# Kernel tuning notes

Hardware: AMD Instinct MI355X
Metric: run time of the kernel (lower is better)

The kernel has to match this reference:

```python
import jax, jax.numpy as jnp
import numpy as np

D = 256  # feature_dim
B, N = 16, 1024
NEG_SLOPE = 0.2
SCALE = float(np.sqrt(D))


def setup_inputs() -> dict:
    key = jax.random.key(0)
    ks = jax.random.split(key, 8)
    s = 1.0 / np.sqrt(D)  # torch Linear default init scale
    return {
        "feature": jax.random.normal(ks[0], (B, N, D), dtype=jnp.float32),
        "graph": jax.random.randint(ks[1], (B, N, N), 0, 2, dtype=jnp.int32),
        "W_w": jax.random.uniform(ks[2], (D, D), jnp.float32, -s, s),
        "W_b": jax.random.uniform(ks[3], (D,), jnp.float32, -s, s),
        "Q_w": jax.random.uniform(ks[4], (D, D), jnp.float32, -s, s),
        "Q_b": jax.random.uniform(ks[5], (D,), jnp.float32, -s, s),
        "K_w": jax.random.uniform(ks[6], (D, D), jnp.float32, -s, s),
        "K_b": jax.random.uniform(ks[7], (D,), jnp.float32, -s, s),
    }


def reference(feature, graph, W_w, W_b, Q_w, Q_b, K_w, K_b):
    # h = W(feature); torch Linear: x @ W.T + b
    h = jnp.einsum('bnd,ed->bne', feature, W_w) + W_b        # [B,N,D]
    q = jnp.einsum('bnd,ed->bne', h, Q_w) + Q_b              # [B,N,D]
    k = jnp.einsum('bnd,ed->bne', h, K_w) + K_b              # [B,N,D]
    e = jnp.einsum('bnd,bmd->bnm', q, k) / SCALE             # [B,N,N]
    e = jnp.where(e >= 0, e, NEG_SLOPE * e)                  # LeakyReLU(0.2)
    e = jnp.where(graph == 0, jnp.float32(-1e9), e)          # mask
    a = jax.nn.softmax(e, axis=2)                            # dropout = identity (eval)
    out = jax.nn.relu(jnp.einsum('bnm,bmd->bnd', a, h))      # [B,N,D]
    return out
```

## Files before the change

kernel.cpp:

```cpp
#include <hip/hip_runtime.h>
#include <hip/hip_bf16.h>
#include <stdint.h>

#define DD 256
#define NB 16
#define NN 1024
#define MTOT (NB * NN)

typedef __attribute__((ext_vector_type(8))) short short8;
typedef __attribute__((ext_vector_type(4))) float f32x4;

__device__ __forceinline__ ushort f2b(float f) {
  uint32_t u = __float_as_uint(f);
  return (ushort)((u + 0x7fffu + ((u >> 16) & 1u)) >> 16);
}

__device__ __forceinline__ void stage_weights(const float* __restrict__ W,
                                              ushort* Wl, int tid) {
  for (int i = 0; i < 64; ++i) {
    int idx4 = i * 256 + tid;
    int row = idx4 >> 6;
    int col0 = (idx4 & 63) << 2;
    float4 v = ((const float4*)W)[idx4];
    ushort4 b4;
    b4.x = f2b(v.x); b4.y = f2b(v.y); b4.z = f2b(v.z); b4.w = f2b(v.w);
    int byte = (row * 512 + col0 * 2) ^ ((row & 7) << 4);
    *(ushort4*)((char*)Wl + byte) = b4;
  }
}

__global__ __launch_bounds__(256, 1) void gemm_fused(
    const float* __restrict__ feature, const float* __restrict__ W_w,
    const float* __restrict__ W_b, const float* __restrict__ Q_w,
    const float* __restrict__ Q_b, const float* __restrict__ K_w,
    const float* __restrict__ K_b, ushort* __restrict__ hT,
    ushort* __restrict__ q, ushort* __restrict__ k) {
  __shared__ ushort Wl[256 * 256];
  const int tid = threadIdx.x;
  const int w = tid >> 6, lane = tid & 63, l15 = lane & 15, hi = lane >> 4;
  const int m0 = blockIdx.x * 64 + w * 16;
  const int arow = m0 + l15;

  stage_weights(W_w, Wl, tid);
  __syncthreads();

  f32x4 acc[16] = {};
#pragma unroll
  for (int kk = 0; kk < 8; ++kk) {
    const int k0 = kk * 32 + hi * 8;
    const float4* ap = (const float4*)(feature + arow * 256 + k0);
    float4 x = ap[0], y = ap[1];
    short8 a;
    a[0] = (short)f2b(x.x); a[1] = (short)f2b(x.y);
    a[2] = (short)f2b(x.z); a[3] = (short)f2b(x.w);
    a[4] = (short)f2b(y.x); a[5] = (short)f2b(y.y);
    a[6] = (short)f2b(y.z); a[7] = (short)f2b(y.w);
#pragma unroll
    for (int et = 0; et < 16; ++et) {
      int er = et * 16 + l15;
      short8 bf = *(const short8*)((const char*)Wl +
                                   ((er * 512 + k0 * 2) ^ ((er & 7) << 4)));
      acc[et] = __builtin_amdgcn_mfma_f32_16x16x32_bf16(a, bf, acc[et], 0, 0, 0);
    }
  }

  ushort hvals[16][4];
#pragma unroll
  for (int et = 0; et < 16; ++et) {
    float bv = W_b[et * 16 + l15];
#pragma unroll
    for (int r = 0; r < 4; ++r) hvals[et][r] = f2b(acc[et][r] + bv);
  }

  __syncthreads();
  ushort* Tl = Wl;
  {
    const int mloc = w * 16 + hi * 4;
#pragma unroll
    for (int et = 0; et < 16; ++et)
#pragma unroll
      for (int r = 0; r < 4; ++r)
        Tl[(et * 16 + l15) * 64 + mloc + r] = hvals[et][r];
  }
  __syncthreads();

  short8 qa[8];
#pragma unroll
  for (int kk = 0; kk < 8; ++kk) {
    const int k0 = kk * 32 + hi * 8;
#pragma unroll
    for (int j = 0; j < 8; ++j)
      qa[kk][j] = (short)Tl[(k0 + j) * 64 + w * 16 + l15];
  }
  {
    const int bidx = blockIdx.x >> 4;
    const int n0 = (blockIdx.x & 15) * 64;
    ushort* dst = hT + bidx * (256 * 1024) + tid * 1024 + n0;
    const uint4* src = (const uint4*)(Tl + tid * 64);
#pragma unroll
    for (int j = 0; j < 8; ++j) ((uint4*)dst)[j] = src[j];
  }
  __syncthreads();

  stage_weights(Q_w, Wl, tid);
  __syncthreads();
#pragma unroll
  for (int et = 0; et < 16; ++et) acc[et] = (f32x4){0.f, 0.f, 0.f, 0.f};
#pragma unroll
  for (int kk = 0; kk < 8; ++kk) {
    const int k0 = kk * 32 + hi * 8;
#pragma unroll
    for (int et = 0; et < 16; ++et) {
      int er = et * 16 + l15;
      short8 bf = *(const short8*)((const char*)Wl +
                                   ((er * 512 + k0 * 2) ^ ((er & 7) << 4)));
      acc[et] = __builtin_amdgcn_mfma_f32_16x16x32_bf16(qa[kk], bf, acc[et], 0, 0, 0);
    }
  }
#pragma unroll
  for (int et = 0; et < 16; ++et) {
    int e = et * 16 + l15;
    float bv = Q_b[e];
#pragma unroll
    for (int r = 0; r < 4; ++r)
      q[(m0 + hi * 4 + r) * 256 + e] = f2b(acc[et][r] + bv);
  }
  __syncthreads();

  stage_weights(K_w, Wl, tid);
  __syncthreads();
#pragma unroll
  for (int et = 0; et < 16; ++et) acc[et] = (f32x4){0.f, 0.f, 0.f, 0.f};
#pragma unroll
  for (int kk = 0; kk < 8; ++kk) {
    const int k0 = kk * 32 + hi * 8;
#pragma unroll
    for (int et = 0; et < 16; ++et) {
      int er = et * 16 + l15;
      short8 bf = *(const short8*)((const char*)Wl +
                                   ((er * 512 + k0 * 2) ^ ((er & 7) << 4)));
      acc[et] = __builtin_amdgcn_mfma_f32_16x16x32_bf16(qa[kk], bf, acc[et], 0, 0, 0);
    }
  }
#pragma unroll
  for (int et = 0; et < 16; ++et) {
    int e = et * 16 + l15;
    float bv = K_b[e];
#pragma unroll
    for (int r = 0; r < 4; ++r)
      k[(m0 + hi * 4 + r) * 256 + e] = f2b(acc[et][r] + bv);
  }
}

#define SM_KT 0
#define SM_HT 32768
#define SM_PL 65536
#define SM_M2 73728
#define SM_CM 74752
#define SM_SZ 75008

__device__ __forceinline__ int pswz(int row, int bytecol) {
  return (row * 64 + bytecol) ^ ((row & 7) << 4) ^ ((row >> 3) << 5);
}

__global__ __launch_bounds__(512, 2) void attn8(
    const ushort* __restrict__ Q, const ushort* __restrict__ Kb,
    const ushort* __restrict__ HT, const int* __restrict__ graph,
    float* __restrict__ out) {
  __shared__ __align__(16) char smem[SM_SZ];
  ushort* Kt = (ushort*)(smem + SM_KT);
  ushort* Ht = (ushort*)(smem + SM_HT);
  ushort* Pl = (ushort*)(smem + SM_PL);
  uint* M2 = (uint*)(smem + SM_M2);
  float* Cm = (float*)(smem + SM_CM);

  const int tid = threadIdx.x;
  const int w = tid >> 6, lane = tid & 63, l15 = lane & 15, hi = lane >> 4;
  const int wg = w >> 1, half = w & 1;
  const int hw = blockIdx.x;
  const int slot = hw >> 3;
  const int b = (hw & 7) * 2 + (slot >> 4);
  const int q0 = (slot & 15) * 64;
  const int qrow_a = q0 + wg * 16 + l15;
  const int qrow_cl = wg * 16 + hi * 4;
  const int* grow_base = graph + (b * 1024 + q0 + w * 8) * 1024 + lane;

  int greg[8];

#pragma unroll
  for (int j = 0; j < 8; ++j) greg[j] = grow_base[j * 1024];

  short8 qf[8];
#pragma unroll
  for (int kk = 0; kk < 8; ++kk)
    qf[kk] = *(const short8*)(Q + (b * 1024 + qrow_a) * 256 + kk * 32 + hi * 8);

#pragma unroll
  for (int j = 0; j < 8; ++j) {
    unsigned long long mm = __ballot(greg[j] != 0);
    if (lane == 0) {
      M2[(w * 8 + j) * 2] = (uint)mm;
      M2[(w * 8 + j) * 2 + 1] = (uint)(mm >> 32);
    }
  }

  float lR[4] = {0.f, 0.f, 0.f, 0.f};
  f32x4 o[16] = {};

  for (int t = 0; t < 16; ++t) {
    const uint* M2c = M2 + (t & 1) * 128;
    uint* M2n = M2 + ((t & 1) ^ 1) * 128;

    __syncthreads();
#pragma unroll
    for (int i = 0; i < 4; ++i) {
      int c = i * 512 + tid;
      int krow = c >> 5, col0 = (c & 31) << 3;
      uint4 v = *(const uint4*)(Kb + (b * 1024 + t * 64 + krow) * 256 + col0);
      *(uint4*)((char*)Kt + ((krow * 512 + col0 * 2) ^ ((krow & 7) << 4))) = v;
    }
#pragma unroll
    for (int i = 0; i < 4; ++i) {
      int c = i * 512 + tid;
      int drow = c >> 3, col0 = (c & 7) << 3;
      uint4 v = *(const uint4*)(HT + b * (256 * 1024) + drow * 1024 + t * 64 + col0);
      *(uint4*)((char*)Ht + ((drow * 128 + col0 * 2) ^ ((drow & 7) << 4))) = v;
    }
    __syncthreads();

    if (t < 15) {
#pragma unroll
      for (int j = 0; j < 8; ++j) greg[j] = grow_base[j * 1024 + (t + 1) * 64];
    }

    f32x4 s[2] = {};
    __builtin_amdgcn_s_setprio(1);
#pragma unroll
    for (int kk = 0; kk < 8; ++kk) {
#pragma unroll
      for (int nt = 0; nt < 2; ++nt) {
        int krow = half * 32 + nt * 16 + l15;
        short8 kf = *(const short8*)((const char*)Kt +
            ((krow * 512 + (kk * 32 + hi * 8) * 2) ^ ((krow & 7) << 4)));
        s[nt] = __builtin_amdgcn_mfma_f32_16x16x32_bf16(qf[kk], kf, s[nt], 0, 0, 0);
      }
    }
    __builtin_amdgcn_s_setprio(0);

    float p[2][4];
#pragma unroll
    for (int r = 0; r < 4; ++r) {
      uint mw = M2c[(qrow_cl + r) * 2 + half];
      float v0 = s[0][r] * 0.0625f; v0 = (v0 >= 0.f) ? v0 : 0.2f * v0;
      float v1 = s[1][r] * 0.0625f; v1 = (v1 >= 0.f) ? v1 : 0.2f * v1;
      float p0 = ((mw >> l15) & 1u) ? __expf(v0) : 0.f;
      float p1 = ((mw >> (16 + l15)) & 1u) ? __expf(v1) : 0.f;
      p[0][r] = p0; p[1][r] = p1;
      lR[r] += p0 + p1;
    }

    ushort* Pw = Pl + w * 512;
#pragma unroll
    for (int nt = 0; nt < 2; ++nt)
#pragma unroll
      for (int r = 0; r < 4; ++r) {
        int row = hi * 4 + r, col = nt * 16 + l15;
        *(ushort*)((char*)Pw + pswz(row, col * 2)) = f2b(p[nt][r]);
      }
    __asm__ volatile("s_waitcnt lgkmcnt(0)" ::: "memory");
    short8 pa = *(const short8*)((const char*)Pw + pswz(l15, hi * 16));

    __builtin_amdgcn_s_setprio(1);
#pragma unroll
    for (int dt = 0; dt < 16; ++dt) {
      int dcol = dt * 16 + l15;
      short8 hf = *(const short8*)((const char*)Ht +
          ((dcol * 128 + (half * 32 + hi * 8) * 2) ^ ((dcol & 7) << 4)));
      o[dt] = __builtin_amdgcn_mfma_f32_16x16x32_bf16(pa, hf, o[dt], 0, 0, 0);
    }
    __builtin_amdgcn_s_setprio(0);

    if (t < 15) {
#pragma unroll
      for (int j = 0; j < 8; ++j) {
        unsigned long long mm = __ballot(greg[j] != 0);
        if (lane == 0) {
          M2n[(w * 8 + j) * 2] = (uint)mm;
          M2n[(w * 8 + j) * 2 + 1] = (uint)(mm >> 32);
        }
      }
    }
  }

#pragma unroll
  for (int r = 0; r < 4; ++r) {
    lR[r] += __shfl_xor(lR[r], 1);
    lR[r] += __shfl_xor(lR[r], 2);
    lR[r] += __shfl_xor(lR[r], 4);
    lR[r] += __shfl_xor(lR[r], 8);
  }

  __syncthreads();
  float* Ob = (float*)smem;
  if (half == 1) {
#pragma unroll
    for (int dt = 0; dt < 16; ++dt)
#pragma unroll
      for (int r = 0; r < 4; ++r) {
        int row = hi * 4 + r;
        int byte = (row * 1024 + (dt * 16 + l15) * 4) ^ ((row & 15) << 6);
        *(float*)((char*)Ob + wg * 16384 + byte) = o[dt][r];
      }
    if (l15 == 0) {
#pragma unroll
      for (int r = 0; r < 4; ++r)
        Cm[wg * 16 + hi * 4 + r] = lR[r];
    }
  }
  __syncthreads();
  if (half == 0) {
#pragma unroll
    for (int r = 0; r < 4; ++r) {
      int rowl = hi * 4 + r;
      float inv = 1.f / (lR[r] + Cm[wg * 16 + rowl]);
      int orow = b * 1024 + q0 + wg * 16 + rowl;
#pragma unroll
      for (int dt = 0; dt < 16; ++dt) {
        int byte = (rowl * 1024 + (dt * 16 + l15) * 4) ^ ((rowl & 15) << 6);
        float ob = *(const float*)((const char*)Ob + wg * 16384 + byte);
        float v = (o[dt][r] + ob) * inv;
        out[orow * 256 + dt * 16 + l15] = fmaxf(v, 0.f);
      }
    }
  }
}

extern "C" void kernel_launch(void* const* d_in, const int* in_sizes, int n_in,
                              void* d_out, int out_size, void* d_ws,
                              size_t ws_size, hipStream_t stream) {
  const float* feature = (const float*)d_in[0];
  const int* graph = (const int*)d_in[1];
  const float* W_w = (const float*)d_in[2];
  const float* W_b = (const float*)d_in[3];
  const float* Q_w = (const float*)d_in[4];
  const float* Q_b = (const float*)d_in[5];
  const float* K_w = (const float*)d_in[6];
  const float* K_b = (const float*)d_in[7];
  float* out = (float*)d_out;

  ushort* hT = (ushort*)d_ws;
  ushort* q = hT + MTOT * DD;
  ushort* k = q + MTOT * DD;

  gemm_fused<<<256, 256, 0, stream>>>(feature, W_w, W_b, Q_w, Q_b, K_w, K_b,
                                      hT, q, k);
  attn8<<<256, 512, 0, stream>>>(q, k, hT, graph, out);
}
```

Before: 93.69 us.

## Load K, H and graph mask directly from global memory, dropping LDS staging

The attention kernel no longer stages K and H^T tiles through shared memory with block-wide barriers. Each wave now reads its MFMA operand fragments straight from global memory (relying on L1/L2), and reads the graph mask per element instead of ballot-packing it into LDS bitmasks. This removes two __syncthreads per tile and the LDS copy traffic, at the cost of redundant global loads across waves, less coalesced 16-byte accesses, and no prefetch overlap for the next tile.

After: 166.2 us. +77.4%, slower.

```diff
diff --git a/kernel.cpp b/kernel.cpp
--- a/kernel.cpp
+++ b/kernel.cpp
@@ -152,12 +152,10 @@
   }
 }
 
-#define SM_KT 0
-#define SM_HT 32768
+#define SM_OB 0
 #define SM_PL 65536
-#define SM_M2 73728
-#define SM_CM 74752
-#define SM_SZ 75008
+#define SM_CM 73728
+#define SM_SZ 73984
 
 __device__ __forceinline__ int pswz(int row, int bytecol) {
   return (row * 64 + bytecol) ^ ((row & 7) << 4) ^ ((row >> 3) << 5);
@@ -168,10 +166,7 @@
     const ushort* __restrict__ HT, const int* __restrict__ graph,
     float* __restrict__ out) {
   __shared__ __align__(16) char smem[SM_SZ];
-  ushort* Kt = (ushort*)(smem + SM_KT);
-  ushort* Ht = (ushort*)(smem + SM_HT);
   ushort* Pl = (ushort*)(smem + SM_PL);
-  uint* M2 = (uint*)(smem + SM_M2);
   float* Cm = (float*)(smem + SM_CM);
 
   const int tid = threadIdx.x;
@@ -183,55 +178,26 @@
   const int q0 = (slot & 15) * 64;
   const int qrow_a = q0 + wg * 16 + l15;
   const int qrow_cl = wg * 16 + hi * 4;
-  const int* grow_base = graph + (b * 1024 + q0 + w * 8) * 1024 + lane;
-
-  int greg[8];
-
-#pragma unroll
-  for (int j = 0; j < 8; ++j) greg[j] = grow_base[j * 1024];
 
   short8 qf[8];
 #pragma unroll
   for (int kk = 0; kk < 8; ++kk)
     qf[kk] = *(const short8*)(Q + (b * 1024 + qrow_a) * 256 + kk * 32 + hi * 8);
 
-#pragma unroll
-  for (int j = 0; j < 8; ++j) {
-    unsigned long long mm = __ballot(greg[j] != 0);
-    if (lane == 0) {
-      M2[(w * 8 + j) * 2] = (uint)mm;
-      M2[(w * 8 + j) * 2 + 1] = (uint)(mm >> 32);
-    }
-  }
+  const ushort* Kbase = Kb + (b * 1024 + half * 32 + l15) * 256 + hi * 8;
+  const ushort* Hbase = HT + b * 262144 + half * 32 + hi * 8;
+  const int* Gbase = graph + (b * 1024 + q0 + qrow_cl) * 1024 + half * 32 + l15;
 
   float lR[4] = {0.f, 0.f, 0.f, 0.f};
   f32x4 o[16] = {};
 
   for (int t = 0; t < 16; ++t) {
-    const uint* M2c = M2 + (t & 1) * 128;
-    uint* M2n = M2 + ((t & 1) ^ 1) * 128;
-
-    __syncthreads();
-#pragma unroll
-    for (int i = 0; i < 4; ++i) {
-      int c = i * 512 + tid;
-      int krow = c >> 5, col0 = (c & 31) << 3;
-      uint4 v = *(const uint4*)(Kb + (b * 1024 + t * 64 + krow) * 256 + col0);
-      *(uint4*)((char*)Kt + ((krow * 512 + col0 * 2) ^ ((krow & 7) << 4))) = v;
-    }
-#pragma unroll
-    for (int i = 0; i < 4; ++i) {
-      int c = i * 512 + tid;
-      int drow = c >> 3, col0 = (c & 7) << 3;
-      uint4 v = *(const uint4*)(HT + b * (256 * 1024) + drow * 1024 + t * 64 + col0);
-      *(uint4*)((char*)Ht + ((drow * 128 + col0 * 2) ^ ((drow & 7) << 4))) = v;
-    }
-    __syncthreads();
-
-    if (t < 15) {
-#pragma unroll
-      for (int j = 0; j < 8; ++j) greg[j] = grow_base[j * 1024 + (t + 1) * 64];
-    }
+    int g[2][4];
+#pragma unroll
+    for (int nt = 0; nt < 2; ++nt)
+#pragma unroll
+      for (int r = 0; r < 4; ++r)
+        g[nt][r] = Gbase[r * 1024 + t * 64 + nt * 16];
 
     f32x4 s[2] = {};
     __builtin_amdgcn_s_setprio(1);
@@ -239,9 +205,7 @@
     for (int kk = 0; kk < 8; ++kk) {
 #pragma unroll
       for (int nt = 0; nt < 2; ++nt) {
-        int krow = half * 32 + nt * 16 + l15;
-        short8 kf = *(const short8*)((const char*)Kt +
-            ((krow * 512 + (kk * 32 + hi * 8) * 2) ^ ((krow & 7) << 4)));
+        short8 kf = *(const short8*)(Kbase + (t * 64 + nt * 16) * 256 + kk * 32);
         s[nt] = __builtin_amdgcn_mfma_f32_16x16x32_bf16(qf[kk], kf, s[nt], 0, 0, 0);
       }
     }
@@ -250,11 +214,10 @@
     float p[2][4];
 #pragma unroll
     for (int r = 0; r < 4; ++r) {
-      uint mw = M2c[(qrow_cl + r) * 2 + half];
       float v0 = s[0][r] * 0.0625f; v0 = (v0 >= 0.f) ? v0 : 0.2f * v0;
       float v1 = s[1][r] * 0.0625f; v1 = (v1 >= 0.f) ? v1 : 0.2f * v1;
-      float p0 = ((mw >> l15) & 1u) ? __expf(v0) : 0.f;
-      float p1 = ((mw >> (16 + l15)) & 1u) ? __expf(v1) : 0.f;
+      float p0 = g[0][r] ? __expf(v0) : 0.f;
+      float p1 = g[1][r] ? __expf(v1) : 0.f;
       p[0][r] = p0; p[1][r] = p1;
       lR[r] += p0 + p1;
     }
@@ -274,22 +237,10 @@
 #pragma unroll
     for (int dt = 0; dt < 16; ++dt) {
       int dcol = dt * 16 + l15;
-      short8 hf = *(const short8*)((const char*)Ht +
-          ((dcol * 128 + (half * 32 + hi * 8) * 2) ^ ((dcol & 7) << 4)));
+      short8 hf = *(const short8*)(Hbase + dcol * 1024 + t * 64);
       o[dt] = __builtin_amdgcn_mfma_f32_16x16x32_bf16(pa, hf, o[dt], 0, 0, 0);
     }
     __builtin_amdgcn_s_setprio(0);
-
-    if (t < 15) {
-#pragma unroll
-      for (int j = 0; j < 8; ++j) {
-        unsigned long long mm = __ballot(greg[j] != 0);
-        if (lane == 0) {
-          M2n[(w * 8 + j) * 2] = (uint)mm;
-          M2n[(w * 8 + j) * 2 + 1] = (uint)(mm >> 32);
-        }
-      }
-    }
   }
 
 #pragma unroll
@@ -300,8 +251,7 @@
     lR[r] += __shfl_xor(lR[r], 8);
   }
 
-  __syncthreads();
-  float* Ob = (float*)smem;
+  float* Ob = (float*)(smem + SM_OB);
   if (half == 1) {
 #pragma unroll
     for (int dt = 0; dt < 16; ++dt)
```

## Process 128 keys per outer iteration with doubled K/H LDS tiles

Applied to the files above, without the earlier changes.

Each outer iteration of the attention kernel now loads two 64-key chunks of K and H^T into separate LDS buffers. It then computes both sub-tiles before the next barrier, which halves the number of __syncthreads and loop iterations. LDS use roughly doubles to about 141KB, so launch bounds drop to one 512-thread block per CU. That reduces occupancy and latency hiding. Graph mask prefetch is widened to match.

After: 110.3 us. 1.18x slower.

```diff
diff --git a/kernel.cpp b/kernel.cpp
--- a/kernel.cpp
+++ b/kernel.cpp
@@ -152,24 +152,24 @@
   }
 }
 
-#define SM_KT 0
-#define SM_HT 32768
-#define SM_PL 65536
-#define SM_M2 73728
-#define SM_CM 74752
-#define SM_SZ 75008
+#define SM_KT0 0
+#define SM_KT1 32768
+#define SM_HT0 65536
+#define SM_HT1 98304
+#define SM_PL 131072
+#define SM_M2 139264
+#define SM_CM 141312
+#define SM_SZ 141568
 
 __device__ __forceinline__ int pswz(int row, int bytecol) {
   return (row * 64 + bytecol) ^ ((row & 7) << 4) ^ ((row >> 3) << 5);
 }
 
-__global__ __launch_bounds__(512, 2) void attn8(
+__global__ __launch_bounds__(512, 1) void attn8(
     const ushort* __restrict__ Q, const ushort* __restrict__ Kb,
     const ushort* __restrict__ HT, const int* __restrict__ graph,
     float* __restrict__ out) {
   __shared__ __align__(16) char smem[SM_SZ];
-  ushort* Kt = (ushort*)(smem + SM_KT);
-  ushort* Ht = (ushort*)(smem + SM_HT);
   ushort* Pl = (ushort*)(smem + SM_PL);
   uint* M2 = (uint*)(smem + SM_M2);
   float* Cm = (float*)(smem + SM_CM);
@@ -185,10 +185,13 @@
   const int qrow_cl = wg * 16 + hi * 4;
   const int* grow_base = graph + (b * 1024 + q0 + w * 8) * 1024 + lane;
 
-  int greg[8];
-
-#pragma unroll
-  for (int j = 0; j < 8; ++j) greg[j] = grow_base[j * 1024];
+  int greg[16];
+
+#pragma unroll
+  for (int j = 0; j < 8; ++j) {
+    greg[j] = grow_base[j * 1024];
+    greg[8 + j] = grow_base[j * 1024 + 64];
+  }
 
   short8 qf[8];
 #pragma unroll
@@ -197,96 +200,119 @@
 
 #pragma unroll
   for (int j = 0; j < 8; ++j) {
-    unsigned long long mm = __ballot(greg[j] != 0);
+    unsigned long long m0 = __ballot(greg[j] != 0);
+    unsigned long long m1 = __ballot(greg[8 + j] != 0);
     if (lane == 0) {
-      M2[(w * 8 + j) * 2] = (uint)mm;
-      M2[(w * 8 + j) * 2 + 1] = (uint)(mm >> 32);
+      M2[(w * 8 + j) * 2] = (uint)m0;
+      M2[(w * 8 + j) * 2 + 1] = (uint)(m0 >> 32);
+      M2[128 + (w * 8 + j) * 2] = (uint)m1;
+      M2[128 + (w * 8 + j) * 2 + 1] = (uint)(m1 >> 32);
     }
   }
 
   float lR[4] = {0.f, 0.f, 0.f, 0.f};
   f32x4 o[16] = {};
 
-  for (int t = 0; t < 16; ++t) {
-    const uint* M2c = M2 + (t & 1) * 128;
-    uint* M2n = M2 + ((t & 1) ^ 1) * 128;
+  for (int t = 0; t < 8; ++t) {
+    const int par = t & 1;
+    const uint* M2cur = M2 + par * 256;
+    uint* M2nxt = M2 + (par ^ 1) * 256;
 
     __syncthreads();
 #pragma unroll
-    for (int i = 0; i < 4; ++i) {
-      int c = i * 512 + tid;
+    for (int i = 0; i < 8; ++i) {
+      int c = (i & 3) * 512 + tid;
+      int kbuf = (i >> 2);
       int krow = c >> 5, col0 = (c & 31) << 3;
-      uint4 v = *(const uint4*)(Kb + (b * 1024 + t * 64 + krow) * 256 + col0);
-      *(uint4*)((char*)Kt + ((krow * 512 + col0 * 2) ^ ((krow & 7) << 4))) = v;
-    }
-#pragma unroll
-    for (int i = 0; i < 4; ++i) {
-      int c = i * 512 + tid;
+      uint4 v = *(const uint4*)(
+          Kb + (b * 1024 + t * 128 + kbuf * 64 + krow) * 256 + col0);
+      *(uint4*)((char*)smem + (kbuf ? SM_KT1 : SM_KT0) +
+                ((krow * 512 + col0 * 2) ^ ((krow & 7) << 4))) = v;
+    }
+#pragma unroll
+    for (int i = 0; i < 8; ++i) {
+      int c = (i & 3) * 512 + tid;
+      int hbuf = (i >> 2);
       int drow = c >> 3, col0 = (c & 7) << 3;
-      uint4 v = *(const uint4*)(HT + b * (256 * 1024) + drow * 1024 + t * 64 + col0);
-      *(uint4*)((char*)Ht + ((drow * 128 + col0 * 2) ^ ((drow & 7) << 4))) = v;
+      uint4 v = *(const uint4*)(HT + b * (256 * 1024) + drow * 1024 +
+                                t * 128 + hbuf * 64 + col0);
+      *(uint4*)((char*)smem + (hbuf ? SM_HT1 : SM_HT0) +
+                ((drow * 128 + col0 * 2) ^ ((drow & 7) << 4))) = v;
     }
     __syncthreads();
 
-    if (t < 15) {
-#pragma unroll
-      for (int j = 0; j < 8; ++j) greg[j] = grow_base[j * 1024 + (t + 1) * 64];
-    }
-
-    f32x4 s[2] = {};
-    __builtin_amdgcn_s_setprio(1);
-#pragma unroll
-    for (int kk = 0; kk < 8; ++kk) {
-#pragma unroll
-      for (int nt = 0; nt < 2; ++nt) {
-        int krow = half * 32 + nt * 16 + l15;
-        short8 kf = *(const short8*)((const char*)Kt +
-            ((krow * 512 + (kk * 32 + hi * 8) * 2) ^ ((krow & 7) << 4)));
-        s[nt] = __builtin_amdgcn_mfma_f32_16x16x32_bf16(qf[kk], kf, s[nt], 0, 0, 0);
-      }
-    }
-    __builtin_amdgcn_s_setprio(0);
-
-    float p[2][4];
-#pragma unroll
-    for (int r = 0; r < 4; ++r) {
-      uint mw = M2c[(qrow_cl + r) * 2 + half];
-      float v0 = s[0][r] * 0.0625f; v0 = (v0 >= 0.f) ? v0 : 0.2f * v0;
-      float v1 = s[1][r] * 0.0625f; v1 = (v1 >= 0.f) ? v1 : 0.2f * v1;
-      float p0 = ((mw >> l15) & 1u) ? __expf(v0) : 0.f;
-      float p1 = ((mw >> (16 + l15)) & 1u) ? __expf(v1) : 0.f;
-      p[0][r] = p0; p[1][r] = p1;
-      lR[r] += p0 + p1;
-    }
-
-    ushort* Pw = Pl + w * 512;
-#pragma unroll
-    for (int nt = 0; nt < 2; ++nt)
+    if (t < 7) {
+#pragma unroll
+      for (int j = 0; j < 8; ++j) {
+        greg[j] = grow_base[j * 1024 + (t + 1) * 128];
+        greg[8 + j] = grow_base[j * 1024 + (t + 1) * 128 + 64];
+      }
+    }
+
+#pragma unroll
+    for (int sub = 0; sub < 2; ++sub) {
+      const ushort* Kt = (const ushort*)(smem + (sub ? SM_KT1 : SM_KT0));
+      const ushort* Ht = (const ushort*)(smem + (sub ? SM_HT1 : SM_HT0));
+      const uint* M2c = M2cur + sub * 128;
+
+      f32x4 s[2] = {};
+      __builtin_amdgcn_s_setprio(1);
+#pragma unroll
+      for (int kk = 0; kk < 8; ++kk) {
+#pragma unroll
+        for (int nt = 0; nt < 2; ++nt) {
+          int krow = half * 32 + nt * 16 + l15;
+          short8 kf = *(const short8*)((const char*)Kt +
+              ((krow * 512 + (kk * 32 + hi * 8) * 2) ^ ((krow & 7) << 4)));
+          s[nt] = __builtin_amdgcn_mfma_f32_16x16x32_bf16(qf[kk], kf, s[nt], 0, 0, 0);
+        }
+      }
+      __builtin_amdgcn_s_setprio(0);
+
+      float p[2][4];
 #pragma unroll
       for (int r = 0; r < 4; ++r) {
-        int row = hi * 4 + r, col = nt * 16 + l15;
-        *(ushort*)((char*)Pw + pswz(row, col * 2)) = f2b(p[nt][r]);
-      }
-    __asm__ volatile("s_waitcnt lgkmcnt(0)" ::: "memory");
-    short8 pa = *(const short8*)((const char*)Pw + pswz(l15, hi * 16));
-
-    __builtin_amdgcn_s_setprio(1);
-#pragma unroll
-    for (int dt = 0; dt < 16; ++dt) {
-      int dcol = dt * 16 + l15;
-      short8 hf = *(const short8*)((const char*)Ht +
-          ((dcol * 128 + (half * 32 + hi * 8) * 2) ^ ((dcol & 7) << 4)));
-      o[dt] = __builtin_amdgcn_mfma_f32_16x16x32_bf16(pa, hf, o[dt], 0, 0, 0);
-    }
-    __builtin_amdgcn_s_setprio(0);
-
-    if (t < 15) {
+        uint mw = M2c[(qrow_cl + r) * 2 + half];
+        float v0 = s[0][r] * 0.0625f; v0 = (v0 >= 0.f) ? v0 : 0.2f * v0;
+        float v1 = s[1][r] * 0.0625f; v1 = (v1 >= 0.f) ? v1 : 0.2f * v1;
+        float p0 = ((mw >> l15) & 1u) ? __expf(v0) : 0.f;
+        float p1 = ((mw >> (16 + l15)) & 1u) ? __expf(v1) : 0.f;
+        p[0][r] = p0; p[1][r] = p1;
+        lR[r] += p0 + p1;
+      }
+
+      ushort* Pw = Pl + w * 512;
+#pragma unroll
+      for (int nt = 0; nt < 2; ++nt)
+#pragma unroll
+        for (int r = 0; r < 4; ++r) {
+          int row = hi * 4 + r, col = nt * 16 + l15;
+          *(ushort*)((char*)Pw + pswz(row, col * 2)) = f2b(p[nt][r]);
+        }
+      __asm__ volatile("s_waitcnt lgkmcnt(0)" ::: "memory");
+      short8 pa = *(const short8*)((const char*)Pw + pswz(l15, hi * 16));
+
+      __builtin_amdgcn_s_setprio(1);
+#pragma unroll
+      for (int dt = 0; dt < 16; ++dt) {
+        int dcol = dt * 16 + l15;
+        short8 hf = *(const short8*)((const char*)Ht +
+            ((dcol * 128 + (half * 32 + hi * 8) * 2) ^ ((dcol & 7) << 4)));
+        o[dt] = __builtin_amdgcn_mfma_f32_16x16x32_bf16(pa, hf, o[dt], 0, 0, 0);
+      }
+      __builtin_amdgcn_s_setprio(0);
+    }
+
+    if (t < 7) {
 #pragma unroll
       for (int j = 0; j < 8; ++j) {
-        unsigned long long mm = __ballot(greg[j] != 0);
+        unsigned long long m0 = __ballot(greg[j] != 0);
+        unsigned long long m1 = __ballot(greg[8 + j] != 0);
         if (lane == 0) {
-          M2n[(w * 8 + j) * 2] = (uint)mm;
-          M2n[(w * 8 + j) * 2 + 1] = (uint)(mm >> 32);
+          M2nxt[(w * 8 + j) * 2] = (uint)m0;
+          M2nxt[(w * 8 + j) * 2 + 1] = (uint)(m0 >> 32);
+          M2nxt[128 + (w * 8 + j) * 2] = (uint)m1;
+          M2nxt[128 + (w * 8 + j) * 2 + 1] = (uint)(m1 >> 32);
         }
       }
     }
```

## Split attention key range across two blocks with atomic accumulation and finalize pass

Applied to the files above, without the earlier changes.

Each attention block now processes only half of the key tiles, which doubles the grid to 512 blocks. Partial numerators go into the output and partial softmax denominators into a workspace buffer, both via float atomicAdd. A new finalize kernel then applies ReLU and the normalization. The launch bound is raised to request higher occupancy. The aim is better CU utilization and latency hiding, at the cost of two memsets, atomic traffic over the whole output, an extra full read/write pass, and non-deterministic summation order.

Measured after the change: 248.2 us. 165% more time.

```diff
diff --git a/kernel.cpp b/kernel.cpp
--- a/kernel.cpp
+++ b/kernel.cpp
@@ -163,10 +163,10 @@
   return (row * 64 + bytecol) ^ ((row & 7) << 4) ^ ((row >> 3) << 5);
 }
 
-__global__ __launch_bounds__(512, 2) void attn8(
+__global__ __launch_bounds__(512, 4) void attn8(
     const ushort* __restrict__ Q, const ushort* __restrict__ Kb,
     const ushort* __restrict__ HT, const int* __restrict__ graph,
-    float* __restrict__ out) {
+    float* __restrict__ out, float* __restrict__ l_acc) {
   __shared__ __align__(16) char smem[SM_SZ];
   ushort* Kt = (ushort*)(smem + SM_KT);
   ushort* Ht = (ushort*)(smem + SM_HT);
@@ -179,11 +179,15 @@
   const int wg = w >> 1, half = w & 1;
   const int hw = blockIdx.x;
   const int slot = hw >> 3;
-  const int b = (hw & 7) * 2 + (slot >> 4);
-  const int q0 = (slot & 15) * 64;
+  const int b = (hw & 7) * 2 + (slot >> 5);
+  const int rest = slot & 31;
+  const int q0 = (rest >> 1) * 64;
+  const int ks = rest & 1;
+  const int kt0 = ks * 8;
   const int qrow_a = q0 + wg * 16 + l15;
   const int qrow_cl = wg * 16 + hi * 4;
-  const int* grow_base = graph + (b * 1024 + q0 + w * 8) * 1024 + lane;
+  const int* grow_base =
+      graph + (b * 1024 + q0 + w * 8) * 1024 + ks * 512 + lane;
 
   int greg[8];
 
@@ -207,28 +211,29 @@
   float lR[4] = {0.f, 0.f, 0.f, 0.f};
   f32x4 o[16] = {};
 
-  for (int t = 0; t < 16; ++t) {
+  for (int t = 0; t < 8; ++t) {
     const uint* M2c = M2 + (t & 1) * 128;
     uint* M2n = M2 + ((t & 1) ^ 1) * 128;
+    const int gk = (kt0 + t) * 64;
 
     __syncthreads();
 #pragma unroll
     for (int i = 0; i < 4; ++i) {
       int c = i * 512 + tid;
       int krow = c >> 5, col0 = (c & 31) << 3;
-      uint4 v = *(const uint4*)(Kb + (b * 1024 + t * 64 + krow) * 256 + col0);
+      uint4 v = *(const uint4*)(Kb + (b * 1024 + gk + krow) * 256 + col0);
       *(uint4*)((char*)Kt + ((krow * 512 + col0 * 2) ^ ((krow & 7) << 4))) = v;
     }
 #pragma unroll
     for (int i = 0; i < 4; ++i) {
       int c = i * 512 + tid;
       int drow = c >> 3, col0 = (c & 7) << 3;
-      uint4 v = *(const uint4*)(HT + b * (256 * 1024) + drow * 1024 + t * 64 + col0);
+      uint4 v = *(const uint4*)(HT + b * (256 * 1024) + drow * 1024 + gk + col0);
       *(uint4*)((char*)Ht + ((drow * 128 + col0 * 2) ^ ((drow & 7) << 4))) = v;
     }
     __syncthreads();
 
-    if (t < 15) {
+    if (t < 7) {
 #pragma unroll
       for (int j = 0; j < 8; ++j) greg[j] = grow_base[j * 1024 + (t + 1) * 64];
     }
@@ -280,7 +285,7 @@
     }
     __builtin_amdgcn_s_setprio(0);
 
-    if (t < 15) {
+    if (t < 7) {
 #pragma unroll
       for (int j = 0; j < 8; ++j) {
         unsigned long long mm = __ballot(greg[j] != 0);
@@ -322,16 +327,32 @@
 #pragma unroll
     for (int r = 0; r < 4; ++r) {
       int rowl = hi * 4 + r;
-      float inv = 1.f / (lR[r] + Cm[wg * 16 + rowl]);
+      float lpart = lR[r] + Cm[wg * 16 + rowl];
       int orow = b * 1024 + q0 + wg * 16 + rowl;
+      if (l15 == 0) atomicAdd(&l_acc[orow], lpart);
 #pragma unroll
       for (int dt = 0; dt < 16; ++dt) {
         int byte = (rowl * 1024 + (dt * 16 + l15) * 4) ^ ((rowl & 15) << 6);
         float ob = *(const float*)((const char*)Ob + wg * 16384 + byte);
-        float v = (o[dt][r] + ob) * inv;
-        out[orow * 256 + dt * 16 + l15] = fmaxf(v, 0.f);
-      }
-    }
+        atomicAdd(&out[orow * 256 + dt * 16 + l15], o[dt][r] + ob);
+      }
+    }
+  }
+}
+
+__global__ __launch_bounds__(256) void finalize(float* __restrict__ out,
+                                                const float* __restrict__ l_acc) {
+  const long i4 = (long)blockIdx.x * blockDim.x + threadIdx.x;
+  const long n4 = (long)MTOT * DD / 4;
+  const long stride = (long)gridDim.x * blockDim.x;
+  for (long i = i4; i < n4; i += stride) {
+    float4 v = ((const float4*)out)[i];
+    float inv = 1.f / l_acc[(i * 4) >> 8];
+    v.x = fmaxf(v.x, 0.f) * inv;
+    v.y = fmaxf(v.y, 0.f) * inv;
+    v.z = fmaxf(v.z, 0.f) * inv;
+    v.w = fmaxf(v.w, 0.f) * inv;
+    ((float4*)out)[i] = v;
   }
 }
 
@@ -351,8 +372,12 @@
   ushort* hT = (ushort*)d_ws;
   ushort* q = hT + MTOT * DD;
   ushort* k = q + MTOT * DD;
-
+  float* l_acc = (float*)(k + MTOT * DD);
+
+  hipMemsetAsync(out, 0, (size_t)MTOT * DD * sizeof(float), stream);
+  hipMemsetAsync(l_acc, 0, (size_t)MTOT * sizeof(float), stream);
   gemm_fused<<<256, 256, 0, stream>>>(feature, W_w, W_b, Q_w, Q_b, K_w, K_b,
                                       hT, q, k);
-  attn8<<<256, 512, 0, stream>>>(q, k, hT, graph, out);
-}
+  attn8<<<512, 512, 0, stream>>>(q, k, hT, graph, out, l_acc);
+  finalize<<<1024, 256, 0, stream>>>(out, l_acc);
+}
```
